# Optimization experiments

Hardware: AMD Instinct MI355X
Metric: run time of the kernel (lower is better)

The kernel has to match this reference:

```python
import jax, jax.numpy as jnp
import numpy as np

T, B, D, H = 512, 8, 512, 8
DH = D // H


def _sinusoidal(pos, dim):
    # pos: (t, t) float relative distances -> (t, t, dim)
    half = dim // 2
    freqs = jnp.exp(-jnp.log(10000.0) * jnp.arange(half, dtype=jnp.float32) / half)
    ang = pos[..., None] * freqs  # (t, t, half)
    return jnp.concatenate([jnp.sin(ang), jnp.cos(ang)], axis=-1)


def setup_inputs() -> dict:
    key = jax.random.key(0)
    ks = jax.random.split(key, 7)
    s = 0.02
    return {
        "x": jax.random.normal(ks[0], (T, B, D), jnp.float32),
        "W_qkv": jax.random.normal(ks[1], (D, 3 * D), jnp.float32) * s,  # to_qkv (no bias)
        "W_pos": jax.random.normal(ks[2], (D, D), jnp.float32) * s,      # to_pos (no bias)
        "pos_u": jax.random.normal(ks[3], (H, DH), jnp.float32),
        "pos_v": jax.random.normal(ks[4], (H, DH), jnp.float32),
        "W_out": jax.random.normal(ks[5], (D, D), jnp.float32) * s,
        "b_out": jnp.zeros((D,), jnp.float32),
        "log_one_div_by_tau": jnp.zeros((1,), jnp.float32),
    }


def reference(x, W_qkv, W_pos, pos_u, pos_v, W_out, b_out, log_one_div_by_tau):
    t, b, d = x.shape
    h, dh = pos_u.shape
    scale = dh ** (-0.5)

    qkv = x @ W_qkv                                   # (t, b, 3d)
    q, k, v = jnp.split(qkv, 3, axis=-1)
    q = q.reshape(t, b, h, dh)
    k = k.reshape(t, b, h, dh)
    v = v.reshape(t, b, h, dh)

    # relative position embeddings
    seq = jnp.arange(t, dtype=jnp.float32)
    rel_dist = seq[:, None] - seq[None, :]            # (t, t)
    rpe = _sinusoidal(rel_dist, d) @ W_pos            # (t, t, d)
    rpe = rpe.reshape(t, t, h, dh)

    # Transformer-XL energy: AC + BD + global content bias + global pos bias
    energy = (
        jnp.einsum('ibhd,jbhd->ijbh', q, k)
        + jnp.einsum('ibhd,ijhd->ijbh', q, rpe)
        + jnp.einsum('hd,jbhd->jbh', pos_u, k)[None, :, :, :]
        + jnp.einsum('hd,ijhd->ijh', pos_v, rpe)[:, :, None, :]
    )
    energy = energy * scale

    # diag mask
    diag = jnp.eye(t, dtype=bool)[:, :, None, None]
    energy = jnp.where(diag, -jnp.finfo(energy.dtype).max, energy)

    # log temperature
    energy = energy * jnp.exp(log_one_div_by_tau)

    attn = jax.nn.softmax(energy, axis=1)             # softmax over j
    out = jnp.einsum('ijbh,jbhd->ibhd', attn, v).reshape(t, b, d)
    return out @ W_out + b_out
```

## Files before the change

kernel.cpp:

```cpp
#include <hip/hip_runtime.h>
#include <hip/hip_bf16.h>

#define TT 512
#define BB 8
#define DD 512
#define HH 8
#define DHH 64

typedef unsigned short ushort_t;
using frag16 = __attribute__((ext_vector_type(8))) short;
using f32x4  = __attribute__((ext_vector_type(4))) float;
using usx4   = __attribute__((ext_vector_type(4))) ushort_t;

#define MFMA16 __builtin_amdgcn_mfma_f32_16x16x32_bf16

__device__ inline ushort_t f2bf(float x) {
    __hip_bfloat16 h = __float2bfloat16(x);
    ushort_t u; __builtin_memcpy(&u, &h, 2); return u;
}
__device__ inline float bf2f(ushort_t u) {
    __hip_bfloat16 h; __builtin_memcpy(&h, &u, 2);
    return __bfloat162float(h);
}

__device__ inline void gload16(const void* g, void* l) {
    __builtin_amdgcn_global_load_lds(
        (const __attribute__((address_space(1))) unsigned int*)g,
        (__attribute__((address_space(3))) unsigned int*)l, 16, 0, 0);
}

__device__ inline void split_t_tile(const float* __restrict__ in,
                                    ushort_t* __restrict__ oh,
                                    ushort_t* __restrict__ ol,
                                    int K, int N, int bx, int by, int tid,
                                    float (*tile)[33]) {
    int n0 = bx * 32, k0 = by * 32;
    {
        int r = tid >> 3, c0 = (tid & 7) * 4;
        float4 v = *(const float4*)&in[(size_t)(k0 + r) * N + n0 + c0];
        tile[r][c0] = v.x; tile[r][c0 + 1] = v.y;
        tile[r][c0 + 2] = v.z; tile[r][c0 + 3] = v.w;
    }
    __syncthreads();
    {
        int n = tid >> 3, kk = (tid & 7) * 4;
        usx4 H, L;
        #pragma unroll
        for (int t = 0; t < 4; ++t) {
            float x = tile[kk + t][n];
            ushort_t hh = f2bf(x);
            H[t] = hh;
            L[t] = f2bf(x - bf2f(hh));
        }
        *(usx4*)&oh[(size_t)(n0 + n) * K + k0 + kk] = H;
        *(usx4*)&ol[(size_t)(n0 + n) * K + k0 + kk] = L;
    }
}

__global__ __launch_bounds__(256) void prep_kernel(
        const float* __restrict__ x, const float* __restrict__ W_pos,
        const float* __restrict__ W_qkv, const float* __restrict__ W_out,
        ushort_t* __restrict__ fh, ushort_t* __restrict__ fl,
        ushort_t* __restrict__ xh,
        ushort_t* __restrict__ WposT_h, ushort_t* __restrict__ WposT_l,
        ushort_t* __restrict__ WqkvT_h, ushort_t* __restrict__ WqkvT_l,
        ushort_t* __restrict__ WoutT_h, ushort_t* __restrict__ WoutT_l) {
    __shared__ float tile[32][33];
    int blk = blockIdx.x;
    int tid = threadIdx.x;
    if (blk < 512) {
        int idx = blk * 1024 + tid * 4;
        int r = idx >> 9, c0 = idx & 511;
        float dist = (float)(r - 511);
        const float nl4 = -logf(10000.0f) / 256.0f;
        usx4 H, L;
        #pragma unroll
        for (int t = 0; t < 4; ++t) {
            int c = c0 + t;
            int cc = c & 255;
            float freq = __expf(nl4 * (float)cc);
            float ang = dist * freq;
            float v = (c < 256) ? __sinf(ang) : __cosf(ang);
            ushort_t hh = f2bf(v);
            H[t] = hh;
            L[t] = f2bf(v - bf2f(hh));
        }
        *(usx4*)&fh[idx] = H;
        *(usx4*)&fl[idx] = L;
    } else if (blk < 2560) {
        int i = (blk - 512) * 256 + tid;
        float4 v = ((const float4*)x)[i];
        float e[4] = {v.x, v.y, v.z, v.w};
        usx4 H;
        #pragma unroll
        for (int t = 0; t < 4; ++t) H[t] = f2bf(e[t]);
        ((usx4*)xh)[i] = H;
    } else if (blk < 2816) {
        int f = blk - 2560;
        split_t_tile(W_pos, WposT_h, WposT_l, 512, 512, f & 15, f >> 4, tid, tile);
    } else if (blk < 3584) {
        int f = blk - 2816;
        split_t_tile(W_qkv, WqkvT_h, WqkvT_l, 512, 1536, f % 48, f / 48, tid, tile);
    } else {
        int f = blk - 3584;
        split_t_tile(W_out, WoutT_h, WoutT_l, 512, 512, f & 15, f >> 4, tid, tile);
    }
}

template <int TM, int TN, int MODE, int APL>
__device__ void gemm_bf3_dev(
        ushort_t* lds0, ushort_t* lds1, int bx, int by,
        const ushort_t* __restrict__ Ah, const ushort_t* __restrict__ Al,
        const ushort_t* __restrict__ Bh, const ushort_t* __restrict__ Bl,
        const float* __restrict__ bias, float* __restrict__ C,
        ushort_t* __restrict__ Ch, ushort_t* __restrict__ Cl,
        int M, int N, int K, int lo_nlim) {
    constexpr int NMI = TM / 32;
    constexpr int NNI = TN / 32;
    constexpr int ACELLS = APL * 4 * TM;
    constexpr int NCH = (ACELLS + 8 * TN) / 64;

    const int tid = threadIdx.x;
    const int lane = tid & 63;
    const int w = tid >> 6;
    const int wm = w & 1, wn = w >> 1;
    const int c = lane & 15, quad = lane >> 4;
    const int m0 = by * TM;
    const int n0 = bx * TN;
    const bool wlo = (MODE == 1) && (n0 < lo_nlim);

    auto stage = [&](int k0, ushort_t* lds) {
        #pragma unroll
        for (int ci = 0; ci < NCH / 4; ++ci) {
            int ch = ci * 4 + w;
            int cell = ch * 64 + lane;
            const ushort_t* src;
            if (cell < ACELLS) {
                int plane = cell / (4 * TM);
                int rem = cell - plane * 4 * TM;
                int q = rem / TM, r = rem - q * TM;
                src = (plane ? Al : Ah) + (size_t)(m0 + r) * K + k0 + q * 8;
            } else {
                int cb = cell - ACELLS;
                int plane = cb / (4 * TN);
                int rem = cb - plane * 4 * TN;
                int q = rem / TN, r = rem - q * TN;
                src = (plane ? Bl : Bh) + (size_t)(n0 + r) * K + k0 + q * 8;
            }
            gload16(src, &lds[(size_t)(ch * 64) * 8]);
        }
    };

    f32x4 acc[NMI][NNI];
    #pragma unroll
    for (int mi = 0; mi < NMI; ++mi)
        #pragma unroll
        for (int ni = 0; ni < NNI; ++ni)
            acc[mi][ni] = (f32x4){0.f, 0.f, 0.f, 0.f};

    const int NIT = K >> 5;
    stage(0, lds0);
    for (int it = 0; it < NIT; ++it) {
        ushort_t* cur = (it & 1) ? lds1 : lds0;
        ushort_t* nxt = (it & 1) ? lds0 : lds1;
        __syncthreads();
        if (it + 1 < NIT) stage((it + 1) * 32, nxt);

        frag16 a_h[NMI], a_l[NMI], b_h[NNI], b_l[NNI];
        #pragma unroll
        for (int mi = 0; mi < NMI; ++mi) {
            int arow = wm * (TM / 2) + mi * 16 + c;
            a_h[mi] = *(const frag16*)&cur[((0 * 4 + quad) * TM + arow) * 8];
            if (APL == 2)
                a_l[mi] = *(const frag16*)&cur[((4 + quad) * TM + arow) * 8];
        }
        #pragma unroll
        for (int ni = 0; ni < NNI; ++ni) {
            int brow = wn * (TN / 2) + ni * 16 + c;
            b_h[ni] = *(const frag16*)&cur[(ACELLS + (0 * 4 + quad) * TN + brow) * 8];
            b_l[ni] = *(const frag16*)&cur[(ACELLS + (4 + quad) * TN + brow) * 8];
        }
        #pragma unroll
        for (int mi = 0; mi < NMI; ++mi)
            #pragma unroll
            for (int ni = 0; ni < NNI; ++ni) {
                acc[mi][ni] = MFMA16(a_h[mi], b_h[ni], acc[mi][ni], 0, 0, 0);
                acc[mi][ni] = MFMA16(a_h[mi], b_l[ni], acc[mi][ni], 0, 0, 0);
                if (APL == 2)
                    acc[mi][ni] = MFMA16(a_l[mi], b_h[ni], acc[mi][ni], 0, 0, 0);
            }
    }

    if constexpr (MODE == 3) {
        __syncthreads();
        ushort_t* tp = lds0;
        #pragma unroll
        for (int mi = 0; mi < NMI; ++mi)
            #pragma unroll
            for (int ni = 0; ni < NNI; ++ni)
                #pragma unroll
                for (int reg = 0; reg < 4; ++reg) {
                    int lm = wm * (TM / 2) + mi * 16 + quad * 4 + reg;
                    int ln = wn * (TN / 2) + ni * 16 + c;
                    tp[lm * 136 + ln] = f2bf(acc[mi][ni][reg]);
                }
        __syncthreads();
        int t0 = m0 >> 3;
        #pragma unroll
        for (int rr = 0; rr < 4; ++rr) {
            int row = tid + rr * 256;
            int bloc = row >> 7, dl = row & 127;
            union { frag16 v; ushort_t s[8]; } P0, P1;
            #pragma unroll
            for (int tl = 0; tl < 8; ++tl)
                P0.s[tl] = tp[(tl * 8 + bloc) * 136 + dl];
            #pragma unroll
            for (int tl = 0; tl < 8; ++tl)
                P1.s[tl] = tp[((tl + 8) * 8 + bloc) * 136 + dl];
            size_t dst = ((size_t)bloc * DD + (n0 - 1024) + dl) * TT + t0;
            *(frag16*)&Ch[dst]     = P0.v;
            *(frag16*)&Ch[dst + 8] = P1.v;
        }
        return;
    }

    #pragma unroll
    for (int mi = 0; mi < NMI; ++mi)
        #pragma unroll
        for (int ni = 0; ni < NNI; ++ni)
            #pragma unroll
            for (int reg = 0; reg < 4; ++reg) {
                int gm = m0 + wm * (TM / 2) + mi * 16 + quad * 4 + reg;
                int gn = n0 + wn * (TN / 2) + ni * 16 + c;
                float v = acc[mi][ni][reg];
                if (MODE == 0) {
                    C[(size_t)gm * N + gn] = v + bias[gn];
                } else {
                    ushort_t hh = f2bf(v);
                    Ch[(size_t)gm * N + gn] = hh;
                    if (MODE == 1 && wlo)
                        Cl[(size_t)gm * N + gn] = f2bf(v - bf2f(hh));
                }
            }
}

__global__ __launch_bounds__(256, 2) void big_gemm(
        const ushort_t* __restrict__ x_h,
        const ushort_t* __restrict__ WqkvT_h, const ushort_t* __restrict__ WqkvT_l,
        ushort_t* __restrict__ qkv_h, ushort_t* __restrict__ qkv_l,
        ushort_t* __restrict__ vt_h,
        const ushort_t* __restrict__ feat_h, const ushort_t* __restrict__ feat_l,
        const ushort_t* __restrict__ WposT_h, const ushort_t* __restrict__ WposT_l,
        ushort_t* __restrict__ table_h) {
    __shared__ __align__(16) ushort_t lds[2 * 12288];
    int blk = blockIdx.x;
    if (blk < 384) {
        int xcd = blk & 7, idx = blk >> 3;
        int bm = xcd * 4 + idx / 12;
        int bn = idx % 12;
        if (bn < 8) {
            gemm_bf3_dev<128, 128, 1, 1>(lds, lds + 12288, bn, bm,
                                         x_h, nullptr, WqkvT_h, WqkvT_l,
                                         nullptr, nullptr, qkv_h, qkv_l,
                                         4096, 1536, 512, 512);
        } else {
            gemm_bf3_dev<128, 128, 3, 1>(lds, lds + 12288, bn, bm,
                                         x_h, nullptr, WqkvT_h, WqkvT_l,
                                         nullptr, nullptr, vt_h, nullptr,
                                         4096, 1536, 512, 0);
        }
    } else {
        int f = blk - 384;
        int xcd = f & 7, idx = f >> 3;
        int bm = xcd * 2 + (idx >> 3);
        int bn = idx & 7;
        gemm_bf3_dev<64, 64, 2, 2>(lds, lds + 8192, bn, bm,
                                   feat_h, feat_l, WposT_h, WposT_l,
                                   nullptr, nullptr, table_h, nullptr,
                                   1024, 512, 512, 0);
    }
}

__global__ __launch_bounds__(256, 3) void outproj_gemm(
        const ushort_t* __restrict__ ao_h, const ushort_t* __restrict__ ao_l,
        const ushort_t* __restrict__ WoutT_h, const ushort_t* __restrict__ WoutT_l,
        const float* __restrict__ bias, float* __restrict__ C) {
    __shared__ __align__(16) ushort_t lds[2 * 8192];
    int blk = blockIdx.x;
    int xcd = blk & 7, idx = blk >> 3;
    int bm = xcd * 8 + (idx >> 3);
    int bn = idx & 7;
    gemm_bf3_dev<64, 64, 0, 2>(lds, lds + 8192, bn, bm,
                               ao_h, ao_l, WoutT_h, WoutT_l,
                               bias, C, nullptr, nullptr,
                               4096, 512, 512, 0);
}

struct WU {
    union {
        float    qp[16][81];
        ushort_t p[16][72];
    };
};

__global__ __launch_bounds__(256, 2) void attn_kernel(
        const ushort_t* __restrict__ qkv_h, const ushort_t* __restrict__ qkv_l,
        const ushort_t* __restrict__ T_h,
        const ushort_t* __restrict__ vt_h,
        const float* __restrict__ pos_u, const float* __restrict__ pos_v,
        const float* __restrict__ tau,
        ushort_t* __restrict__ o_h, ushort_t* __restrict__ o_l) {
    const int b  = blockIdx.x;
    const int i0 = blockIdx.y * 64;
    const int h  = blockIdx.z;
    const int tid  = threadIdx.x;
    const int lane = tid & 63;
    const int w    = tid >> 6;
    const int c    = lane & 15;
    const int quad = lane >> 4;

    __shared__ __align__(16) ushort_t Kbuf[2][4096];
    __shared__ __align__(16) ushort_t Vbuf[2][4096];
    __shared__ __align__(16) ushort_t Pbuf[192 * 64];
    __shared__ __align__(16) WU wbuf[4];

    const int chl = (lane & 7) ^ (lane >> 3);
    const int rql = lane >> 3;
    const int swz0 = quad ^ (c & 7);
    const int swz1 = (4 + quad) ^ (c & 7);

    const float tauexp = expf(tau[0]);
    const float scale  = 0.125f;
    const float NEGMAX = -3.4028234663852886e38f;

    frag16 qu_h[2], qu_l[2], qv_h[2], qv_l[2];
    {
        int row = i0 + w * 16 + c;
        size_t base = ((size_t)row * BB + b) * (3 * DD) + h * DHH;
        const float* up = pos_u + h * DHH;
        const float* vp = pos_v + h * DHH;
        #pragma unroll
        for (int kb = 0; kb < 2; ++kb) {
            int d0 = kb * 32 + quad * 8;
            union { frag16 v; ushort_t s[8]; } QH, QL, UH, UL, VH, VL;
            QH.v = *(const frag16*)&qkv_h[base + d0];
            QL.v = *(const frag16*)&qkv_l[base + d0];
            #pragma unroll
            for (int t = 0; t < 8; ++t) {
                float q = bf2f(QH.s[t]) + bf2f(QL.s[t]);
                float a = q + up[d0 + t];
                ushort_t ah = f2bf(a);
                UH.s[t] = ah; UL.s[t] = f2bf(a - bf2f(ah));
                float bq = q + vp[d0 + t];
                ushort_t bh = f2bf(bq);
                VH.s[t] = bh; VL.s[t] = f2bf(bq - bf2f(bh));
            }
            qu_h[kb] = UH.v; qu_l[kb] = UL.v;
            qv_h[kb] = VH.v; qv_l[kb] = VL.v;
        }
    }

    auto stageKV = [&](int jt) {
        const int j0 = jt * 64;
        ushort_t* kb = Kbuf[jt & 1];
        ushort_t* vb = Vbuf[jt & 1];
        #pragma unroll
        for (int it = 0; it < 2; ++it) {
            int r0 = (it * 4 + w) * 8;
            const ushort_t* src = qkv_h
                + ((size_t)(j0 + r0 + rql) * BB + b) * (3 * DD) + DD + h * DHH + chl * 8;
            gload16(src, &kb[r0 * 64]);
        }
        #pragma unroll
        for (int it = 0; it < 2; ++it) {
            int r0 = (it * 4 + w) * 8;
            const ushort_t* src = vt_h
                + ((size_t)b * DD + h * DHH + r0 + rql) * TT + j0 + chl * 8;
            gload16(src, &vb[r0 * 64]);
        }
    };
    auto stageP = [&](int rbase, int nit) {
        for (int it = 0; it < nit; ++it) {
            int row = rbase + (it * 4 + w) * 8;
            int sbase = row % 192;
            const ushort_t* src = T_h + (size_t)(row + rql) * DD + h * DHH + chl * 8;
            gload16(src, &Pbuf[sbase * 64]);
        }
    };

    float m_r[4], l_r[4];
    f32x4 o_acc[4];
    #pragma unroll
    for (int r = 0; r < 4; ++r) { m_r[r] = NEGMAX; l_r[r] = 0.f; }
    #pragma unroll
    for (int d = 0; d < 4; ++d) o_acc[d] = (f32x4){0.f, 0.f, 0.f, 0.f};

    stageKV(0);
    stageP(i0 + 448, 4);

    for (int jt = 0; jt < 8; ++jt) {
        const int j0  = jt * 64;
        const int rlo = i0 - j0 + 448;

        __syncthreads();

        if (jt + 1 < 8) {
            stageKV(jt + 1);
            stageP(rlo - 64, 2);
        }
        const ushort_t* kbc = Kbuf[jt & 1];
        const ushort_t* vbc = Vbuf[jt & 1];

        f32x4 qp_acc[5];
        __builtin_amdgcn_s_setprio(1);
        #pragma unroll
        for (int rs = 0; rs < 5; ++rs) {
            f32x4 acc = (f32x4){0.f, 0.f, 0.f, 0.f};
            int slot = (rlo + w * 16 + rs * 16 + c) % 192;
            frag16 p0 = *(const frag16*)&Pbuf[slot * 64 + swz0 * 8];
            frag16 p1 = *(const frag16*)&Pbuf[slot * 64 + swz1 * 8];
            acc = MFMA16(qv_h[0], p0, acc, 0, 0, 0);
            acc = MFMA16(qv_l[0], p0, acc, 0, 0, 0);
            acc = MFMA16(qv_h[1], p1, acc, 0, 0, 0);
            acc = MFMA16(qv_l[1], p1, acc, 0, 0, 0);
            qp_acc[rs] = acc;
        }
        __builtin_amdgcn_s_setprio(0);
        #pragma unroll
        for (int rs = 0; rs < 5; ++rs)
            #pragma unroll
            for (int reg = 0; reg < 4; ++reg)
                wbuf[w].qp[quad * 4 + reg][rs * 16 + c] = qp_acc[rs][reg];

        f32x4 ac[4];
        __builtin_amdgcn_s_setprio(1);
        #pragma unroll
        for (int js = 0; js < 4; ++js) {
            f32x4 acc = (f32x4){0.f, 0.f, 0.f, 0.f};
            int krow = js * 16 + c;
            frag16 kh0 = *(const frag16*)&kbc[krow * 64 + swz0 * 8];
            frag16 kh1 = *(const frag16*)&kbc[krow * 64 + swz1 * 8];
            acc = MFMA16(qu_h[0], kh0, acc, 0, 0, 0);
            acc = MFMA16(qu_l[0], kh0, acc, 0, 0, 0);
            acc = MFMA16(qu_h[1], kh1, acc, 0, 0, 0);
            acc = MFMA16(qu_l[1], kh1, acc, 0, 0, 0);
            ac[js] = acc;
        }
        __builtin_amdgcn_s_setprio(0);

        float ev[4][4];
        #pragma unroll
        for (int js = 0; js < 4; ++js) {
            int jl = js * 16 + c;
            #pragma unroll
            for (int reg = 0; reg < 4; ++reg) {
                int il = quad * 4 + reg;
                float bd = wbuf[w].qp[il][il - jl + 63];
                float e = (ac[js][reg] + bd) * scale;
                if (i0 + w * 16 + il == j0 + jl) e = NEGMAX;
                ev[js][reg] = e * tauexp;
            }
        }

        float alpha[4], mn[4];
        #pragma unroll
        for (int reg = 0; reg < 4; ++reg) {
            float mx = fmaxf(fmaxf(ev[0][reg], ev[1][reg]),
                             fmaxf(ev[2][reg], ev[3][reg]));
            #pragma unroll
            for (int m = 1; m < 16; m <<= 1) mx = fmaxf(mx, __shfl_xor(mx, m));
            float m2 = fmaxf(m_r[reg], mx);
            alpha[reg] = __expf(m_r[reg] - m2);
            mn[reg] = m2;
            m_r[reg] = m2;
        }
        float ss[4] = {0.f, 0.f, 0.f, 0.f};
        #pragma unroll
        for (int js = 0; js < 4; ++js) {
            int jl = js * 16 + c;
            #pragma unroll
            for (int reg = 0; reg < 4; ++reg) {
                float p = __expf(ev[js][reg] - mn[reg]);
                ushort_t ph = f2bf(p);
                ss[reg] += bf2f(ph);
                wbuf[w].p[quad * 4 + reg][jl] = ph;
            }
        }
        #pragma unroll
        for (int reg = 0; reg < 4; ++reg) {
            float s = ss[reg];
            #pragma unroll
            for (int m = 1; m < 16; m <<= 1) s += __shfl_xor(s, m);
            l_r[reg] = l_r[reg] * alpha[reg] + s;
        }

        frag16 pf0 = *(const frag16*)&wbuf[w].p[c][quad * 8];
        frag16 pf1 = *(const frag16*)&wbuf[w].p[c][32 + quad * 8];
        __builtin_amdgcn_s_setprio(1);
        #pragma unroll
        for (int ds = 0; ds < 4; ++ds) {
            f32x4 acc = o_acc[ds];
            #pragma unroll
            for (int reg = 0; reg < 4; ++reg) acc[reg] *= alpha[reg];
            int vrow = ds * 16 + c;
            frag16 vh0 = *(const frag16*)&vbc[vrow * 64 + swz0 * 8];
            frag16 vh1 = *(const frag16*)&vbc[vrow * 64 + swz1 * 8];
            acc = MFMA16(pf0, vh0, acc, 0, 0, 0);
            acc = MFMA16(pf1, vh1, acc, 0, 0, 0);
            o_acc[ds] = acc;
        }
        __builtin_amdgcn_s_setprio(0);
    }

    #pragma unroll
    for (int reg = 0; reg < 4; ++reg)
        l_r[reg] = __builtin_amdgcn_rcpf(l_r[reg]);
    #pragma unroll
    for (int ds = 0; ds < 4; ++ds)
        #pragma unroll
        for (int reg = 0; reg < 4; ++reg) {
            int row = i0 + w * 16 + quad * 4 + reg;
            size_t idx = ((size_t)row * BB + b) * DD + h * DHH + ds * 16 + c;
            float val = o_acc[ds][reg] * l_r[reg];
            ushort_t hh = f2bf(val);
            o_h[idx] = hh;
            o_l[idx] = f2bf(val - bf2f(hh));
        }
}

extern "C" void kernel_launch(void* const* d_in, const int* in_sizes, int n_in,
                              void* d_out, int out_size, void* d_ws, size_t ws_size,
                              hipStream_t stream) {
    const float* x     = (const float*)d_in[0];
    const float* W_qkv = (const float*)d_in[1];
    const float* W_pos = (const float*)d_in[2];
    const float* pos_u = (const float*)d_in[3];
    const float* pos_v = (const float*)d_in[4];
    const float* W_out = (const float*)d_in[5];
    const float* b_out = (const float*)d_in[6];
    const float* tau   = (const float*)d_in[7];
    float* out = (float*)d_out;

    ushort_t* p = (ushort_t*)d_ws;
    ushort_t* feat_h  = p; p += 1024 * 512;
    ushort_t* feat_l  = p; p += 1024 * 512;
    ushort_t* WposT_h = p; p += 512 * 512;
    ushort_t* WposT_l = p; p += 512 * 512;
    ushort_t* table_h = p; p += 1024 * 512;
    ushort_t* x_h     = p; p += 4096 * 512;
    ushort_t* WqkvT_h = p; p += 1536 * 512;
    ushort_t* WqkvT_l = p; p += 1536 * 512;
    ushort_t* qkv_h   = p; p += 4096 * 1536;
    ushort_t* qkv_l   = p; p += 4096 * 1536;
    ushort_t* WoutT_h = p; p += 512 * 512;
    ushort_t* WoutT_l = p; p += 512 * 512;
    ushort_t* ao_h    = p; p += 4096 * 512;
    ushort_t* ao_l    = p; p += 4096 * 512;
    ushort_t* vt_h    = p; p += BB * DD * TT;

    prep_kernel<<<3840, 256, 0, stream>>>(
        x, W_pos, W_qkv, W_out, feat_h, feat_l, x_h,
        WposT_h, WposT_l, WqkvT_h, WqkvT_l, WoutT_h, WoutT_l);
    big_gemm<<<512, 256, 0, stream>>>(
        x_h, WqkvT_h, WqkvT_l, qkv_h, qkv_l, vt_h,
        feat_h, feat_l, WposT_h, WposT_l, table_h);
    attn_kernel<<<dim3(BB, 8, HH), 256, 0, stream>>>(
        qkv_h, qkv_l, table_h, vt_h, pos_u, pos_v, tau, ao_h, ao_l);
    outproj_gemm<<<512, 256, 0, stream>>>(
        ao_h, ao_l, WoutT_h, WoutT_l, b_out, out);
}
```

Before: 153.2 us.

## Deepen K-tile to 64 for small GEMMs and replace modulo ring-slot indexing

Adds a BK template parameter so the 64x64 pos-table and out-projection GEMMs stage 64-wide K slices per iteration, halving the number of barriers and pipeline steps at the cost of doubled LDS buffers. The out-projection kernel's occupancy hint drops from 3 to 2 blocks to fit the larger shared memory. In the attention kernel, the per-access modulo-192 ring-buffer slot computation is replaced by an incrementally maintained offset with conditional subtraction, which removes integer divisions from the inner loop.

```diff
diff --git a/kernel.cpp b/kernel.cpp
--- a/kernel.cpp
+++ b/kernel.cpp
@@ -107,7 +107,7 @@
     }
 }
 
-template <int TM, int TN, int MODE, int APL>
+template <int TM, int TN, int MODE, int APL, int BK>
 __device__ void gemm_bf3_dev(
         ushort_t* lds0, ushort_t* lds1, int bx, int by,
         const ushort_t* __restrict__ Ah, const ushort_t* __restrict__ Al,
@@ -117,8 +117,10 @@
         int M, int N, int K, int lo_nlim) {
     constexpr int NMI = TM / 32;
     constexpr int NNI = TN / 32;
-    constexpr int ACELLS = APL * 4 * TM;
-    constexpr int NCH = (ACELLS + 8 * TN) / 64;
+    constexpr int CHK = BK / 8;
+    constexpr int ACELLS = APL * CHK * TM;
+    constexpr int BCELLS = 2 * CHK * TN;
+    constexpr int NCH = (ACELLS + BCELLS) / 64;
 
     const int tid = threadIdx.x;
     const int lane = tid & 63;
@@ -136,14 +138,14 @@
             int cell = ch * 64 + lane;
             const ushort_t* src;
             if (cell < ACELLS) {
-                int plane = cell / (4 * TM);
-                int rem = cell - plane * 4 * TM;
+                int plane = cell / (CHK * TM);
+                int rem = cell - plane * CHK * TM;
                 int q = rem / TM, r = rem - q * TM;
                 src = (plane ? Al : Ah) + (size_t)(m0 + r) * K + k0 + q * 8;
             } else {
                 int cb = cell - ACELLS;
-                int plane = cb / (4 * TN);
-                int rem = cb - plane * 4 * TN;
+                int plane = cb / (CHK * TN);
+                int rem = cb - plane * CHK * TN;
                 int q = rem / TN, r = rem - q * TN;
                 src = (plane ? Bl : Bh) + (size_t)(n0 + r) * K + k0 + q * 8;
             }
@@ -158,37 +160,40 @@
         for (int ni = 0; ni < NNI; ++ni)
             acc[mi][ni] = (f32x4){0.f, 0.f, 0.f, 0.f};
 
-    const int NIT = K >> 5;
+    const int NIT = K / BK;
     stage(0, lds0);
     for (int it = 0; it < NIT; ++it) {
         ushort_t* cur = (it & 1) ? lds1 : lds0;
         ushort_t* nxt = (it & 1) ? lds0 : lds1;
         __syncthreads();
-        if (it + 1 < NIT) stage((it + 1) * 32, nxt);
-
-        frag16 a_h[NMI], a_l[NMI], b_h[NNI], b_l[NNI];
-        #pragma unroll
-        for (int mi = 0; mi < NMI; ++mi) {
-            int arow = wm * (TM / 2) + mi * 16 + c;
-            a_h[mi] = *(const frag16*)&cur[((0 * 4 + quad) * TM + arow) * 8];
-            if (APL == 2)
-                a_l[mi] = *(const frag16*)&cur[((4 + quad) * TM + arow) * 8];
-        }
-        #pragma unroll
-        for (int ni = 0; ni < NNI; ++ni) {
-            int brow = wn * (TN / 2) + ni * 16 + c;
-            b_h[ni] = *(const frag16*)&cur[(ACELLS + (0 * 4 + quad) * TN + brow) * 8];
-            b_l[ni] = *(const frag16*)&cur[(ACELLS + (4 + quad) * TN + brow) * 8];
-        }
-        #pragma unroll
-        for (int mi = 0; mi < NMI; ++mi)
+        if (it + 1 < NIT) stage((it + 1) * BK, nxt);
+
+        #pragma unroll
+        for (int ks = 0; ks < BK / 32; ++ks) {
+            frag16 a_h[NMI], a_l[NMI], b_h[NNI], b_l[NNI];
+            #pragma unroll
+            for (int mi = 0; mi < NMI; ++mi) {
+                int arow = wm * (TM / 2) + mi * 16 + c;
+                a_h[mi] = *(const frag16*)&cur[((ks * 4 + quad) * TM + arow) * 8];
+                if (APL == 2)
+                    a_l[mi] = *(const frag16*)&cur[((CHK + ks * 4 + quad) * TM + arow) * 8];
+            }
             #pragma unroll
             for (int ni = 0; ni < NNI; ++ni) {
-                acc[mi][ni] = MFMA16(a_h[mi], b_h[ni], acc[mi][ni], 0, 0, 0);
-                acc[mi][ni] = MFMA16(a_h[mi], b_l[ni], acc[mi][ni], 0, 0, 0);
-                if (APL == 2)
-                    acc[mi][ni] = MFMA16(a_l[mi], b_h[ni], acc[mi][ni], 0, 0, 0);
-            }
+                int brow = wn * (TN / 2) + ni * 16 + c;
+                b_h[ni] = *(const frag16*)&cur[(ACELLS + (ks * 4 + quad) * TN + brow) * 8];
+                b_l[ni] = *(const frag16*)&cur[(ACELLS + (CHK + ks * 4 + quad) * TN + brow) * 8];
+            }
+            #pragma unroll
+            for (int mi = 0; mi < NMI; ++mi)
+                #pragma unroll
+                for (int ni = 0; ni < NNI; ++ni) {
+                    acc[mi][ni] = MFMA16(a_h[mi], b_h[ni], acc[mi][ni], 0, 0, 0);
+                    acc[mi][ni] = MFMA16(a_h[mi], b_l[ni], acc[mi][ni], 0, 0, 0);
+                    if (APL == 2)
+                        acc[mi][ni] = MFMA16(a_l[mi], b_h[ni], acc[mi][ni], 0, 0, 0);
+                }
+        }
     }
 
     if constexpr (MODE == 3) {
@@ -252,48 +257,48 @@
         const ushort_t* __restrict__ feat_h, const ushort_t* __restrict__ feat_l,
         const ushort_t* __restrict__ WposT_h, const ushort_t* __restrict__ WposT_l,
         ushort_t* __restrict__ table_h) {
-    __shared__ __align__(16) ushort_t lds[2 * 12288];
+    __shared__ __align__(16) ushort_t lds[2 * 16384];
     int blk = blockIdx.x;
     if (blk < 384) {
         int xcd = blk & 7, idx = blk >> 3;
         int bm = xcd * 4 + idx / 12;
         int bn = idx % 12;
         if (bn < 8) {
-            gemm_bf3_dev<128, 128, 1, 1>(lds, lds + 12288, bn, bm,
-                                         x_h, nullptr, WqkvT_h, WqkvT_l,
-                                         nullptr, nullptr, qkv_h, qkv_l,
-                                         4096, 1536, 512, 512);
+            gemm_bf3_dev<128, 128, 1, 1, 32>(lds, lds + 12288, bn, bm,
+                                             x_h, nullptr, WqkvT_h, WqkvT_l,
+                                             nullptr, nullptr, qkv_h, qkv_l,
+                                             4096, 1536, 512, 512);
         } else {
-            gemm_bf3_dev<128, 128, 3, 1>(lds, lds + 12288, bn, bm,
-                                         x_h, nullptr, WqkvT_h, WqkvT_l,
-                                         nullptr, nullptr, vt_h, nullptr,
-                                         4096, 1536, 512, 0);
+            gemm_bf3_dev<128, 128, 3, 1, 32>(lds, lds + 12288, bn, bm,
+                                             x_h, nullptr, WqkvT_h, WqkvT_l,
+                                             nullptr, nullptr, vt_h, nullptr,
+                                             4096, 1536, 512, 0);
         }
     } else {
         int f = blk - 384;
         int xcd = f & 7, idx = f >> 3;
         int bm = xcd * 2 + (idx >> 3);
         int bn = idx & 7;
-        gemm_bf3_dev<64, 64, 2, 2>(lds, lds + 8192, bn, bm,
-                                   feat_h, feat_l, WposT_h, WposT_l,
-                                   nullptr, nullptr, table_h, nullptr,
-                                   1024, 512, 512, 0);
-    }
-}
-
-__global__ __launch_bounds__(256, 3) void outproj_gemm(
+        gemm_bf3_dev<64, 64, 2, 2, 64>(lds, lds + 16384, bn, bm,
+                                       feat_h, feat_l, WposT_h, WposT_l,
+                                       nullptr, nullptr, table_h, nullptr,
+                                       1024, 512, 512, 0);
+    }
+}
+
+__global__ __launch_bounds__(256, 2) void outproj_gemm(
         const ushort_t* __restrict__ ao_h, const ushort_t* __restrict__ ao_l,
         const ushort_t* __restrict__ WoutT_h, const ushort_t* __restrict__ WoutT_l,
         const float* __restrict__ bias, float* __restrict__ C) {
-    __shared__ __align__(16) ushort_t lds[2 * 8192];
+    __shared__ __align__(16) ushort_t lds[2 * 16384];
     int blk = blockIdx.x;
     int xcd = blk & 7, idx = blk >> 3;
     int bm = xcd * 8 + (idx >> 3);
     int bn = idx & 7;
-    gemm_bf3_dev<64, 64, 0, 2>(lds, lds + 8192, bn, bm,
-                               ao_h, ao_l, WoutT_h, WoutT_l,
-                               bias, C, nullptr, nullptr,
-                               4096, 512, 512, 0);
+    gemm_bf3_dev<64, 64, 0, 2, 64>(lds, lds + 16384, bn, bm,
+                                   ao_h, ao_l, WoutT_h, WoutT_l,
+                                   bias, C, nullptr, nullptr,
+                                   4096, 512, 512, 0);
 }
 
 struct WU {
@@ -379,11 +384,12 @@
             gload16(src, &vb[r0 * 64]);
         }
     };
-    auto stageP = [&](int rbase, int nit) {
+    auto stageP = [&](int rowbase, int slotbase, int nit) {
         for (int it = 0; it < nit; ++it) {
-            int row = rbase + (it * 4 + w) * 8;
-            int sbase = row % 192;
-            const ushort_t* src = T_h + (size_t)(row + rql) * DD + h * DHH + chl * 8;
+            int off = (it * 4 + w) * 8;
+            int sbase = slotbase + off;
+            if (sbase >= 192) sbase -= 192;
+            const ushort_t* src = T_h + (size_t)(rowbase + off + rql) * DD + h * DHH + chl * 8;
             gload16(src, &Pbuf[sbase * 64]);
         }
     };
@@ -395,18 +401,20 @@
     #pragma unroll
     for (int d = 0; d < 4; ++d) o_acc[d] = (f32x4){0.f, 0.f, 0.f, 0.f};
 
+    int rmod = (i0 + 448) % 192;
     stageKV(0);
-    stageP(i0 + 448, 4);
+    stageP(i0 + 448, rmod, 4);
 
     for (int jt = 0; jt < 8; ++jt) {
         const int j0  = jt * 64;
         const int rlo = i0 - j0 + 448;
+        const int rmodN = (rmod >= 64) ? rmod - 64 : rmod + 128;
 
         __syncthreads();
 
         if (jt + 1 < 8) {
             stageKV(jt + 1);
-            stageP(rlo - 64, 2);
+            stageP(rlo - 64, rmodN, 2);
         }
         const ushort_t* kbc = Kbuf[jt & 1];
         const ushort_t* vbc = Vbuf[jt & 1];
@@ -416,7 +424,8 @@
         #pragma unroll
         for (int rs = 0; rs < 5; ++rs) {
             f32x4 acc = (f32x4){0.f, 0.f, 0.f, 0.f};
-            int slot = (rlo + w * 16 + rs * 16 + c) % 192;
+            int slot = rmod + w * 16 + rs * 16 + c;
+            if (slot >= 192) slot -= 192;
             frag16 p0 = *(const frag16*)&Pbuf[slot * 64 + swz0 * 8];
             frag16 p1 = *(const frag16*)&Pbuf[slot * 64 + swz1 * 8];
             acc = MFMA16(qv_h[0], p0, acc, 0, 0, 0);
@@ -510,6 +519,8 @@
             o_acc[ds] = acc;
         }
         __builtin_amdgcn_s_setprio(0);
+
+        rmod = rmodN;
     }
 
     #pragma unroll
```

Measured after the change: 153.8 us. No clear change (+0.4%).
